# Kernel tuning notes

Measured on AMD Instinct MI355X. Metric: run time of the kernel, lower is better.

The kernel has to match this reference:

```python
import jax, jax.numpy as jnp
import numpy as np

INPUT_DIM = 1024
HIDDEN_DIM = 512
SEQ_LEN = 512


def setup_inputs() -> dict:
    key = jax.random.key(0)
    ks = jax.random.split(key, 7)
    s = 1.0 / np.sqrt(INPUT_DIM)
    s2 = 1.0 / np.sqrt(HIDDEN_DIM)
    return {
        "vectors": jax.random.normal(ks[0], (1, SEQ_LEN, INPUT_DIM), dtype=jnp.float32),
        "W_h": jax.random.uniform(ks[1], (HIDDEN_DIM, INPUT_DIM), jnp.float32, -s, s),
        "b_h": jax.random.uniform(ks[2], (HIDDEN_DIM,), jnp.float32, -s, s),
        "W_m": jax.random.uniform(ks[3], (HIDDEN_DIM, INPUT_DIM), jnp.float32, -s, s),
        "b_m": jax.random.uniform(ks[4], (HIDDEN_DIM,), jnp.float32, -s, s),
        "w2": jax.random.uniform(ks[5], (HIDDEN_DIM,), jnp.float32, -s2, s2),
        "b2": jax.random.uniform(ks[6], (), jnp.float32, -s2, s2),
    }


def reference(vectors, W_h, b_h, W_m, b_m, w2, b2):
    # vectors: [1, S, D] -> squeeze leading batch dim (matches torch .squeeze(0))
    x = vectors[0]  # [S, D]
    # Two batched GEMMs replacing the per-token Python loop
    H = x @ W_h.T + b_h  # [S, Hd] head representations
    M = x @ W_m.T + b_m  # [S, Hd] modifier representations
    # Pairwise broadcast add + tanh + dot with layer_2 weights -> [S, S] scores
    pair = jnp.tanh(H[:, None, :] + M[None, :, :])  # [S, S, Hd]
    scores = jnp.einsum('hmd,d->hm', pair, w2) + b2
    return scores
```

## Files before the change

kernel.cpp:

```cpp
#include <hip/hip_runtime.h>

#define C2 2.8853900817779268f

__device__ __forceinline__ float rcp_fast(float x){ return __builtin_amdgcn_rcpf(x); }
__device__ __forceinline__ float exp2_fast(float x){ return __builtin_amdgcn_exp2f(x); }

__global__ __launch_bounds__(512) void prep_kernel(
    const float* __restrict__ w2, const float* __restrict__ b2,
    float* __restrict__ w2s, float* __restrict__ c0)
{
    int t = threadIdx.x;
    float v = w2[t];
    w2s[t] = -2.0f * v;
    #pragma unroll
    for (int off = 32; off; off >>= 1) v += __shfl_down(v, off, 64);
    __shared__ float part[8];
    if ((t & 63) == 0) part[t >> 6] = v;
    __syncthreads();
    if (t == 0) {
        float s = b2[0];
        #pragma unroll
        for (int i = 0; i < 8; i++) s += part[i];
        *c0 = s;
    }
}

template<int KLEN, bool FINAL>
__global__ __launch_bounds__(128) void gemm_kernel(
    const float* __restrict__ x,
    const float* __restrict__ Wh, const float* __restrict__ bh,
    const float* __restrict__ Wm, const float* __restrict__ bm,
    float* __restrict__ EH, float* __restrict__ EM,
    float* __restrict__ P)
{
    int bz = blockIdx.z;
    int mat   = FINAL ? bz : (bz >> 2);
    int slice = FINAL ? 0  : (bz & 3);
    int k0base = slice * KLEN;
    const float* W = mat ? Wm : Wh;
    int s0 = blockIdx.y * 32;
    int j0 = blockIdx.x * 64;
    __shared__ float Xs[32][33];
    __shared__ float Ws[64][33];
    int tid = threadIdx.x;
    int tx = tid & 15, ty = tid >> 4;
    float acc[4][4] = {};
    for (int kc = 0; kc < KLEN; kc += 32) {
        int k0 = k0base + kc;
        #pragma unroll
        for (int l = 0; l < 2; l++) {
            int slot = tid + l * 128;
            int row = slot >> 3, kq = slot & 7;
            float4 v = *(const float4*)(x + (s0 + row) * 1024 + k0 + kq * 4);
            Xs[row][kq*4+0] = v.x; Xs[row][kq*4+1] = v.y;
            Xs[row][kq*4+2] = v.z; Xs[row][kq*4+3] = v.w;
        }
        #pragma unroll
        for (int l = 0; l < 4; l++) {
            int slot = tid + l * 128;
            int row = slot >> 3, kq = slot & 7;
            float4 v = *(const float4*)(W + (j0 + row) * 1024 + k0 + kq * 4);
            Ws[row][kq*4+0] = v.x; Ws[row][kq*4+1] = v.y;
            Ws[row][kq*4+2] = v.z; Ws[row][kq*4+3] = v.w;
        }
        __syncthreads();
        #pragma unroll 8
        for (int k = 0; k < 32; k++) {
            float a[4], b[4];
            #pragma unroll
            for (int i = 0; i < 4; i++) a[i] = Xs[ty*4+i][k];
            #pragma unroll
            for (int j = 0; j < 4; j++) b[j] = Ws[tx*4+j][k];
            #pragma unroll
            for (int i = 0; i < 4; i++)
                #pragma unroll
                for (int j = 0; j < 4; j++)
                    acc[i][j] = fmaf(a[i], b[j], acc[i][j]);
        }
        __syncthreads();
    }
    if (FINAL) {
        const float* bias = mat ? bm : bh;
        float* O = mat ? EM : EH;
        #pragma unroll
        for (int i = 0; i < 4; i++) {
            int r = s0 + ty*4 + i;
            #pragma unroll
            for (int j = 0; j < 4; j++) {
                int c = j0 + tx*4 + j;
                O[r*512 + c] = exp2_fast(C2 * (acc[i][j] + bias[c]));
            }
        }
    } else {
        float* Pp = P + (size_t)(mat*4 + slice) * (512*512);
        #pragma unroll
        for (int i = 0; i < 4; i++) {
            int r = s0 + ty*4 + i;
            #pragma unroll
            for (int j = 0; j < 4; j++) {
                int c = j0 + tx*4 + j;
                Pp[r*512 + c] = acc[i][j];
            }
        }
    }
}

__global__ __launch_bounds__(256) void finalize_kernel(
    const float* __restrict__ P,
    const float* __restrict__ bh, const float* __restrict__ bm,
    float* __restrict__ EH, float* __restrict__ EM)
{
    int g = blockIdx.x * 256 + threadIdx.x;
    int mat = g >> 18;
    int idx = g & 262143;
    int col = idx & 511;
    const float* Pp = P + (size_t)mat * 4 * 262144 + idx;
    float s = Pp[0] + Pp[262144] + Pp[2*262144] + Pp[3*262144];
    s += (mat ? bm : bh)[col];
    (mat ? EM : EH)[idx] = exp2_fast(C2 * s);
}

__global__ __launch_bounds__(512) void scores_kernel(
    const float* __restrict__ EH, const float* __restrict__ EM,
    const float* __restrict__ w2s, const float* __restrict__ c0,
    float* __restrict__ out)
{
    int m0 = blockIdx.x * 32;
    int h0 = blockIdx.y * 32;
    int tid = threadIdx.x;
    int tx = tid & 31;
    int ty = tid >> 5;
    __shared__ float Hs[32][65];
    __shared__ float Ms[32][65];
    __shared__ float ws_s[64];
    float acc0 = 0.f, acc1 = 0.f;
    for (int d0 = 0; d0 < 512; d0 += 64) {
        {
            int row = tid >> 4;
            int q = tid & 15;
            float4 v = *(const float4*)(EH + (h0 + row) * 512 + d0 + q * 4);
            Hs[row][q*4+0] = v.x; Hs[row][q*4+1] = v.y;
            Hs[row][q*4+2] = v.z; Hs[row][q*4+3] = v.w;
            float4 u = *(const float4*)(EM + (m0 + row) * 512 + d0 + q * 4);
            Ms[row][q*4+0] = u.x; Ms[row][q*4+1] = u.y;
            Ms[row][q*4+2] = u.z; Ms[row][q*4+3] = u.w;
            if (tid < 16) {
                float4 w = *(const float4*)(w2s + d0 + tid * 4);
                ws_s[tid*4+0] = w.x; ws_s[tid*4+1] = w.y;
                ws_s[tid*4+2] = w.z; ws_s[tid*4+3] = w.w;
            }
        }
        __syncthreads();
        #pragma unroll 8
        for (int dk = 0; dk < 64; dk++) {
            float w  = ws_s[dk];
            float em = Ms[tx][dk];
            float e0 = Hs[ty*2+0][dk] * em;
            float e1 = Hs[ty*2+1][dk] * em;
            acc0 = fmaf(w, rcp_fast(e0 + 1.0f), acc0);
            acc1 = fmaf(w, rcp_fast(e1 + 1.0f), acc1);
        }
        __syncthreads();
    }
    float c = *c0;
    out[(h0 + ty*2 + 0) * 512 + m0 + tx] = acc0 + c;
    out[(h0 + ty*2 + 1) * 512 + m0 + tx] = acc1 + c;
}

extern "C" void kernel_launch(void* const* d_in, const int* in_sizes, int n_in,
                              void* d_out, int out_size, void* d_ws, size_t ws_size,
                              hipStream_t stream) {
    const float* x   = (const float*)d_in[0];
    const float* Wh  = (const float*)d_in[1];
    const float* bh  = (const float*)d_in[2];
    const float* Wm  = (const float*)d_in[3];
    const float* bm  = (const float*)d_in[4];
    const float* w2  = (const float*)d_in[5];
    const float* b2  = (const float*)d_in[6];
    float* out = (float*)d_out;

    float* w = (float*)d_ws;
    float* EH  = w;
    float* EM  = w + 262144;
    float* w2s = w + 524288;
    float* c0  = w + 524800;
    float* P   = w + 524864;
    const size_t need_split  = (size_t)(524864 + 8*262144) * 4;
    const size_t need_direct = (size_t)524864 * 4;
    (void)need_direct; (void)in_sizes; (void)n_in; (void)out_size;

    prep_kernel<<<1, 512, 0, stream>>>(w2, b2, w2s, c0);

    if (ws_size >= need_split) {
        gemm_kernel<256, false><<<dim3(8, 16, 8), 128, 0, stream>>>(
            x, Wh, bh, Wm, bm, EH, EM, P);
        finalize_kernel<<<2048, 256, 0, stream>>>(P, bh, bm, EH, EM);
    } else {
        gemm_kernel<1024, true><<<dim3(8, 16, 2), 128, 0, stream>>>(
            x, Wh, bh, Wm, bm, EH, EM, P);
    }

    scores_kernel<<<dim3(16, 16), 512, 0, stream>>>(EH, EM, w2s, c0, out);
}
```

Baseline: 123.4 us.

## Rewrite pipeline with larger GEMM tiles, split-D scores, and combine pass

The GEMM now uses 128x128 tiles with 8x8 per-thread register blocking, an XOR-swizzled shared-memory layout, register prefetch of the next K chunk, and an 8-way split-K. The scores kernel splits the hidden dimension across 8 z-slices with 4x4 register tiles and vectorized LDS reads, writing partials that a new combine kernel reduces and offsets by the bias constant. The prep kernel is folded into the scores and combine kernels. This raises parallelism and reuse in the rcp-bound scores stage. In exchange it needs a much larger workspace (16+8 partial planes) with no size check, and adds extra global traffic for the partial sums.

Result: slower. 318.1 us (+157.7%).

```diff
diff --git a/kernel.cpp b/kernel.cpp
--- a/kernel.cpp
+++ b/kernel.cpp
@@ -1,170 +1,190 @@
 #include <hip/hip_runtime.h>
 
 #define C2 2.8853900817779268f
+#define DIN 1024
+#define HD 512
 
 __device__ __forceinline__ float rcp_fast(float x){ return __builtin_amdgcn_rcpf(x); }
 __device__ __forceinline__ float exp2_fast(float x){ return __builtin_amdgcn_exp2f(x); }
 
-__global__ __launch_bounds__(512) void prep_kernel(
-    const float* __restrict__ w2, const float* __restrict__ b2,
-    float* __restrict__ w2s, float* __restrict__ c0)
-{
-    int t = threadIdx.x;
-    float v = w2[t];
-    w2s[t] = -2.0f * v;
-    #pragma unroll
-    for (int off = 32; off; off >>= 1) v += __shfl_down(v, off, 64);
-    __shared__ float part[8];
-    if ((t & 63) == 0) part[t >> 6] = v;
-    __syncthreads();
-    if (t == 0) {
-        float s = b2[0];
-        #pragma unroll
-        for (int i = 0; i < 8; i++) s += part[i];
-        *c0 = s;
-    }
-}
-
-template<int KLEN, bool FINAL>
-__global__ __launch_bounds__(128) void gemm_kernel(
-    const float* __restrict__ x,
-    const float* __restrict__ Wh, const float* __restrict__ bh,
-    const float* __restrict__ Wm, const float* __restrict__ bm,
-    float* __restrict__ EH, float* __restrict__ EM,
-    float* __restrict__ P)
-{
-    int bz = blockIdx.z;
-    int mat   = FINAL ? bz : (bz >> 2);
-    int slice = FINAL ? 0  : (bz & 3);
-    int k0base = slice * KLEN;
+__global__ __launch_bounds__(256) void gemm_kernel(
+    const float* __restrict__ x, const float* __restrict__ Wh,
+    const float* __restrict__ Wm, float* __restrict__ P)
+{
+    int mat = blockIdx.z >> 3, slice = blockIdx.z & 7;
     const float* W = mat ? Wm : Wh;
-    int s0 = blockIdx.y * 32;
-    int j0 = blockIdx.x * 64;
-    __shared__ float Xs[32][33];
-    __shared__ float Ws[64][33];
+    int s0 = blockIdx.y * 128, j0 = blockIdx.x * 128;
+    int k0base = slice * 128;
+    __shared__ float Xs[128*32];
+    __shared__ float Ws[128*32];
     int tid = threadIdx.x;
     int tx = tid & 15, ty = tid >> 4;
+
+    float4 xr[4], wr[4];
+    auto load_chunk = [&](int c){
+        int k0 = k0base + c*32;
+        #pragma unroll
+        for (int l = 0; l < 4; l++){
+            int row = (tid>>3) + 32*l, q = tid & 7;
+            xr[l] = *(const float4*)(x + (s0+row)*DIN + k0 + q*4);
+            wr[l] = *(const float4*)(W + (j0+row)*DIN + k0 + q*4);
+        }
+    };
+    auto store_chunk = [&](){
+        #pragma unroll
+        for (int l = 0; l < 4; l++){
+            int row = (tid>>3) + 32*l, q = tid & 7;
+            int idx = row*32 + ((q ^ ((row>>3)&7))<<2);
+            *(float4*)&Xs[idx] = xr[l];
+            *(float4*)&Ws[idx] = wr[l];
+        }
+    };
+
+    float acc[8][8] = {};
+    load_chunk(0);
+    for (int c = 0; c < 4; c++){
+        __syncthreads();
+        store_chunk();
+        __syncthreads();
+        if (c < 3) load_chunk(c+1);
+        #pragma unroll
+        for (int qk = 0; qk < 8; qk++){
+            float4 a4[8], b4[8];
+            #pragma unroll
+            for (int i = 0; i < 8; i++)
+                a4[i] = *(const float4*)&Xs[(ty*8+i)*32 + ((qk ^ (ty&7))<<2)];
+            #pragma unroll
+            for (int j = 0; j < 8; j++)
+                b4[j] = *(const float4*)&Ws[(tx*8+j)*32 + ((qk ^ (tx&7))<<2)];
+            #pragma unroll
+            for (int i = 0; i < 8; i++)
+                #pragma unroll
+                for (int j = 0; j < 8; j++){
+                    acc[i][j] = fmaf(a4[i].x, b4[j].x, acc[i][j]);
+                    acc[i][j] = fmaf(a4[i].y, b4[j].y, acc[i][j]);
+                    acc[i][j] = fmaf(a4[i].z, b4[j].z, acc[i][j]);
+                    acc[i][j] = fmaf(a4[i].w, b4[j].w, acc[i][j]);
+                }
+        }
+    }
+    float4* P4 = (float4*)P + (size_t)(mat*8 + slice) * 65536;
+    #pragma unroll
+    for (int i = 0; i < 8; i++){
+        int r = s0 + ty*8 + i;
+        float4 v0 = {acc[i][0], acc[i][1], acc[i][2], acc[i][3]};
+        float4 v1 = {acc[i][4], acc[i][5], acc[i][6], acc[i][7]};
+        P4[r*128 + (j0>>2) + tx*2]     = v0;
+        P4[r*128 + (j0>>2) + tx*2 + 1] = v1;
+    }
+}
+
+__global__ __launch_bounds__(256) void finalize_kernel(
+    const float* __restrict__ P, const float* __restrict__ bh,
+    const float* __restrict__ bm, float* __restrict__ EH, float* __restrict__ EM)
+{
+    int g = blockIdx.x * 256 + threadIdx.x;
+    int mat = g >> 16;
+    int r4 = g & 65535;
+    int col4 = r4 & 127;
+    const float4* P4 = (const float4*)P + (size_t)mat * 8 * 65536;
+    float4 a = P4[r4];
+    #pragma unroll
+    for (int sl = 1; sl < 8; sl++){
+        float4 b = P4[sl*65536 + r4];
+        a.x += b.x; a.y += b.y; a.z += b.z; a.w += b.w;
+    }
+    float4 bias = ((const float4*)(mat ? bm : bh))[col4];
+    float4 e = { exp2_fast(C2*(a.x+bias.x)), exp2_fast(C2*(a.y+bias.y)),
+                 exp2_fast(C2*(a.z+bias.z)), exp2_fast(C2*(a.w+bias.w)) };
+    ((float4*)(mat ? EM : EH))[r4] = e;
+}
+
+__global__ __launch_bounds__(256) void scores_kernel(
+    const float* __restrict__ EH, const float* __restrict__ EM,
+    const float* __restrict__ w2, float* __restrict__ Q)
+{
+    int m0 = blockIdx.x * 64, h0 = blockIdx.y * 64, d0 = blockIdx.z * 64;
+    __shared__ float Hs[64*68];
+    __shared__ float Ms[64*68];
+    __shared__ float wsS[64];
+    int tid = threadIdx.x;
+    int tx = tid & 15, ty = tid >> 4;
+    #pragma unroll
+    for (int l = 0; l < 4; l++){
+        int slot = tid + 256*l;
+        int row = slot >> 4, q = slot & 15;
+        float4 h = *(const float4*)(EH + (h0+row)*HD + d0 + q*4);
+        *(float4*)&Hs[row*68 + q*4] = h;
+        float4 m = *(const float4*)(EM + (m0+row)*HD + d0 + q*4);
+        Ms[(q*4+0)*68 + row] = m.x;
+        Ms[(q*4+1)*68 + row] = m.y;
+        Ms[(q*4+2)*68 + row] = m.z;
+        Ms[(q*4+3)*68 + row] = m.w;
+    }
+    if (tid < 16){
+        float4 w = *(const float4*)(w2 + d0 + tid*4);
+        float4 ws = {-2.f*w.x, -2.f*w.y, -2.f*w.z, -2.f*w.w};
+        *(float4*)&wsS[tid*4] = ws;
+    }
+    __syncthreads();
     float acc[4][4] = {};
-    for (int kc = 0; kc < KLEN; kc += 32) {
-        int k0 = k0base + kc;
-        #pragma unroll
-        for (int l = 0; l < 2; l++) {
-            int slot = tid + l * 128;
-            int row = slot >> 3, kq = slot & 7;
-            float4 v = *(const float4*)(x + (s0 + row) * 1024 + k0 + kq * 4);
-            Xs[row][kq*4+0] = v.x; Xs[row][kq*4+1] = v.y;
-            Xs[row][kq*4+2] = v.z; Xs[row][kq*4+3] = v.w;
-        }
-        #pragma unroll
-        for (int l = 0; l < 4; l++) {
-            int slot = tid + l * 128;
-            int row = slot >> 3, kq = slot & 7;
-            float4 v = *(const float4*)(W + (j0 + row) * 1024 + k0 + kq * 4);
-            Ws[row][kq*4+0] = v.x; Ws[row][kq*4+1] = v.y;
-            Ws[row][kq*4+2] = v.z; Ws[row][kq*4+3] = v.w;
-        }
-        __syncthreads();
-        #pragma unroll 8
-        for (int k = 0; k < 32; k++) {
-            float a[4], b[4];
-            #pragma unroll
-            for (int i = 0; i < 4; i++) a[i] = Xs[ty*4+i][k];
-            #pragma unroll
-            for (int j = 0; j < 4; j++) b[j] = Ws[tx*4+j][k];
-            #pragma unroll
-            for (int i = 0; i < 4; i++)
-                #pragma unroll
-                for (int j = 0; j < 4; j++)
-                    acc[i][j] = fmaf(a[i], b[j], acc[i][j]);
-        }
-        __syncthreads();
-    }
-    if (FINAL) {
-        const float* bias = mat ? bm : bh;
-        float* O = mat ? EM : EH;
-        #pragma unroll
-        for (int i = 0; i < 4; i++) {
-            int r = s0 + ty*4 + i;
-            #pragma unroll
-            for (int j = 0; j < 4; j++) {
-                int c = j0 + tx*4 + j;
-                O[r*512 + c] = exp2_fast(C2 * (acc[i][j] + bias[c]));
+    #pragma unroll
+    for (int it = 0; it < 16; it++){
+        int dk = it*4;
+        float4 w4 = *(const float4*)&wsS[dk];
+        float4 h4[4], mm[4];
+        #pragma unroll
+        for (int i = 0; i < 4; i++)  h4[i] = *(const float4*)&Hs[(ty*4+i)*68 + dk];
+        #pragma unroll
+        for (int dd = 0; dd < 4; dd++) mm[dd] = *(const float4*)&Ms[(dk+dd)*68 + tx*4];
+        #pragma unroll
+        for (int dd = 0; dd < 4; dd++){
+            float w  = (dd==0)?w4.x:(dd==1)?w4.y:(dd==2)?w4.z:w4.w;
+            float4 mv = mm[dd];
+            #pragma unroll
+            for (int i = 0; i < 4; i++){
+                float eh = (dd==0)?h4[i].x:(dd==1)?h4[i].y:(dd==2)?h4[i].z:h4[i].w;
+                acc[i][0] = fmaf(w, rcp_fast(fmaf(eh, mv.x, 1.0f)), acc[i][0]);
+                acc[i][1] = fmaf(w, rcp_fast(fmaf(eh, mv.y, 1.0f)), acc[i][1]);
+                acc[i][2] = fmaf(w, rcp_fast(fmaf(eh, mv.z, 1.0f)), acc[i][2]);
+                acc[i][3] = fmaf(w, rcp_fast(fmaf(eh, mv.w, 1.0f)), acc[i][3]);
             }
         }
-    } else {
-        float* Pp = P + (size_t)(mat*4 + slice) * (512*512);
-        #pragma unroll
-        for (int i = 0; i < 4; i++) {
-            int r = s0 + ty*4 + i;
-            #pragma unroll
-            for (int j = 0; j < 4; j++) {
-                int c = j0 + tx*4 + j;
-                Pp[r*512 + c] = acc[i][j];
-            }
-        }
-    }
-}
-
-__global__ __launch_bounds__(256) void finalize_kernel(
-    const float* __restrict__ P,
-    const float* __restrict__ bh, const float* __restrict__ bm,
-    float* __restrict__ EH, float* __restrict__ EM)
-{
-    int g = blockIdx.x * 256 + threadIdx.x;
-    int mat = g >> 18;
-    int idx = g & 262143;
-    int col = idx & 511;
-    const float* Pp = P + (size_t)mat * 4 * 262144 + idx;
-    float s = Pp[0] + Pp[262144] + Pp[2*262144] + Pp[3*262144];
-    s += (mat ? bm : bh)[col];
-    (mat ? EM : EH)[idx] = exp2_fast(C2 * s);
-}
-
-__global__ __launch_bounds__(512) void scores_kernel(
-    const float* __restrict__ EH, const float* __restrict__ EM,
-    const float* __restrict__ w2s, const float* __restrict__ c0,
-    float* __restrict__ out)
-{
-    int m0 = blockIdx.x * 32;
-    int h0 = blockIdx.y * 32;
+    }
+    float4* Q4 = (float4*)(Q + (size_t)blockIdx.z * 262144);
+    #pragma unroll
+    for (int i = 0; i < 4; i++){
+        float4 v = {acc[i][0], acc[i][1], acc[i][2], acc[i][3]};
+        Q4[(h0 + ty*4 + i)*128 + (m0>>2) + tx] = v;
+    }
+}
+
+__global__ __launch_bounds__(256) void combine_kernel(
+    const float* __restrict__ Q, const float* __restrict__ w2,
+    const float* __restrict__ b2, float* __restrict__ out)
+{
     int tid = threadIdx.x;
-    int tx = tid & 31;
-    int ty = tid >> 5;
-    __shared__ float Hs[32][65];
-    __shared__ float Ms[32][65];
-    __shared__ float ws_s[64];
-    float acc0 = 0.f, acc1 = 0.f;
-    for (int d0 = 0; d0 < 512; d0 += 64) {
-        {
-            int row = tid >> 4;
-            int q = tid & 15;
-            float4 v = *(const float4*)(EH + (h0 + row) * 512 + d0 + q * 4);
-            Hs[row][q*4+0] = v.x; Hs[row][q*4+1] = v.y;
-            Hs[row][q*4+2] = v.z; Hs[row][q*4+3] = v.w;
-            float4 u = *(const float4*)(EM + (m0 + row) * 512 + d0 + q * 4);
-            Ms[row][q*4+0] = u.x; Ms[row][q*4+1] = u.y;
-            Ms[row][q*4+2] = u.z; Ms[row][q*4+3] = u.w;
-            if (tid < 16) {
-                float4 w = *(const float4*)(w2s + d0 + tid * 4);
-                ws_s[tid*4+0] = w.x; ws_s[tid*4+1] = w.y;
-                ws_s[tid*4+2] = w.z; ws_s[tid*4+3] = w.w;
-            }
-        }
-        __syncthreads();
-        #pragma unroll 8
-        for (int dk = 0; dk < 64; dk++) {
-            float w  = ws_s[dk];
-            float em = Ms[tx][dk];
-            float e0 = Hs[ty*2+0][dk] * em;
-            float e1 = Hs[ty*2+1][dk] * em;
-            acc0 = fmaf(w, rcp_fast(e0 + 1.0f), acc0);
-            acc1 = fmaf(w, rcp_fast(e1 + 1.0f), acc1);
-        }
-        __syncthreads();
-    }
-    float c = *c0;
-    out[(h0 + ty*2 + 0) * 512 + m0 + tx] = acc0 + c;
-    out[(h0 + ty*2 + 1) * 512 + m0 + tx] = acc1 + c;
+    __shared__ float red[4];
+    __shared__ float c0s;
+    float s = 0.f;
+    if (tid < 128){ float4 v = ((const float4*)w2)[tid]; s = v.x+v.y+v.z+v.w; }
+    #pragma unroll
+    for (int off = 32; off; off >>= 1) s += __shfl_down(s, off, 64);
+    if (tid < 128 && (tid & 63) == 0) red[tid>>6] = s;
+    __syncthreads();
+    if (tid == 0) c0s = red[0] + red[1] + b2[0];
+    __syncthreads();
+    float c0 = c0s;
+    int g = blockIdx.x * 256 + tid;
+    const float4* Q4 = (const float4*)Q;
+    float4 a = Q4[g];
+    #pragma unroll
+    for (int sl = 1; sl < 8; sl++){
+        float4 b = Q4[sl*65536 + g];
+        a.x += b.x; a.y += b.y; a.z += b.z; a.w += b.w;
+    }
+    float4 o = {a.x + c0, a.y + c0, a.z + c0, a.w + c0};
+    ((float4*)out)[g] = o;
 }
 
 extern "C" void kernel_launch(void* const* d_in, const int* in_sizes, int n_in,
@@ -178,27 +198,16 @@
     const float* w2  = (const float*)d_in[5];
     const float* b2  = (const float*)d_in[6];
     float* out = (float*)d_out;
-
-    float* w = (float*)d_ws;
-    float* EH  = w;
-    float* EM  = w + 262144;
-    float* w2s = w + 524288;
-    float* c0  = w + 524800;
-    float* P   = w + 524864;
-    const size_t need_split  = (size_t)(524864 + 8*262144) * 4;
-    const size_t need_direct = (size_t)524864 * 4;
-    (void)need_direct; (void)in_sizes; (void)n_in; (void)out_size;
-
-    prep_kernel<<<1, 512, 0, stream>>>(w2, b2, w2s, c0);
-
-    if (ws_size >= need_split) {
-        gemm_kernel<256, false><<<dim3(8, 16, 8), 128, 0, stream>>>(
-            x, Wh, bh, Wm, bm, EH, EM, P);
-        finalize_kernel<<<2048, 256, 0, stream>>>(P, bh, bm, EH, EM);
-    } else {
-        gemm_kernel<1024, true><<<dim3(8, 16, 2), 128, 0, stream>>>(
-            x, Wh, bh, Wm, bm, EH, EM, P);
-    }
-
-    scores_kernel<<<dim3(16, 16), 512, 0, stream>>>(EH, EM, w2s, c0, out);
-}
+    (void)in_sizes; (void)n_in; (void)out_size; (void)ws_size;
+
+    float* w  = (float*)d_ws;
+    float* EH = w;
+    float* EM = w + 262144;
+    float* P  = w + 524288;
+    float* Q  = w + 524288 + 16*262144;
+
+    gemm_kernel<<<dim3(4, 4, 16), 256, 0, stream>>>(x, Wh, Wm, P);
+    finalize_kernel<<<512, 256, 0, stream>>>(P, bh, bm, EH, EM);
+    scores_kernel<<<dim3(8, 8, 8), 256, 0, stream>>>(EH, EM, w2, Q);
+    combine_kernel<<<256, 256, 0, stream>>>(Q, w2, b2, out);
+}
```
